# Performance work log

Measured on AMD Instinct MI355X. Metric: run time of the kernel, lower is better.

Reference implementation:

```python
import jax, jax.numpy as jnp
import numpy as np

L = 2          # MPblock_layers
H = 64         # hidden_channels
B, N, E = 1, 50000, 800000


def setup_inputs() -> dict:
    key = jax.random.key(0)
    ks = jax.random.split(key, 12)
    s = 0.05
    return {
        "x": jax.random.normal(ks[0], (B, N, H), jnp.float32),
        "edge_attr": jax.random.normal(ks[1], (B, E, H), jnp.float32),
        "edge_index": jax.random.randint(ks[2], (2, E), 0, N, jnp.int64 if jax.config.jax_enable_x64 else jnp.int32),
        # per-layer stacked MLP params: edge MLP (3H->H->H), node MLP (2H->H->H)
        "edge_w1": jax.random.normal(ks[3], (L, 3 * H, H), jnp.float32) * s,
        "edge_b1": jnp.zeros((L, H), jnp.float32),
        "edge_w2": jax.random.normal(ks[4], (L, H, H), jnp.float32) * s,
        "edge_b2": jnp.zeros((L, H), jnp.float32),
        "node_w1": jax.random.normal(ks[5], (L, 2 * H, H), jnp.float32) * s,
        "node_b1": jnp.zeros((L, H), jnp.float32),
        "node_w2": jax.random.normal(ks[6], (L, H, H), jnp.float32) * s,
        "node_b2": jnp.zeros((L, H), jnp.float32),
    }


def reference(x, edge_attr, edge_index,
              edge_w1, edge_b1, edge_w2, edge_b2,
              node_w1, node_b1, node_w2, node_b2):
    src = edge_index[0]
    dest = edge_index[1]
    n_nodes = x.shape[1]
    for l in range(L):
        # EdgeModel: cat([edge_attr, x[src], x[dest]]) -> MLP
        cat_e = jnp.concatenate([edge_attr, x[:, src], x[:, dest]], axis=2)  # [B,E,3H]
        h = jax.nn.silu(jnp.einsum('bef,fh->beh', cat_e, edge_w1[l]) + edge_b1[l])
        edge_attr = jnp.einsum('beh,hk->bek', h, edge_w2[l]) + edge_b2[l]      # [B,E,H]
        # NodeModel: scatter_add over dest, cat with x, MLP
        agg = jnp.zeros((x.shape[0], n_nodes, edge_attr.shape[2]), x.dtype).at[:, dest].add(edge_attr)
        cat_n = jnp.concatenate([x, agg], axis=2)                              # [B,N,2H]
        h = jax.nn.silu(jnp.einsum('bnf,fh->bnh', cat_n, node_w1[l]) + node_b1[l])
        x = jnp.einsum('bnh,hk->bnk', h, node_w2[l]) + node_b2[l]              # [B,N,H]
    return (x, edge_attr)
```

## Files before the change

### kernel.cpp

```cpp
#include <hip/hip_runtime.h>

typedef __attribute__((ext_vector_type(8))) _Float16 f16x8;
typedef __attribute__((ext_vector_type(4))) _Float16 f16x4;
typedef __attribute__((ext_vector_type(4))) float f32x4;

#define PWS 72

__device__ __forceinline__ float silu_f(float v) {
    return v * (1.0f / (1.0f + __expf(-v)));
}

__device__ __forceinline__ int xcd_swz(int bid, int nwg) {
    if (nwg < 16) return bid;
    int q = nwg >> 3, r = nwg & 7;
    int x = bid & 7, i = bid >> 3;
    int basex = (x < r) ? x * (q + 1) : r * (q + 1) + (x - r) * q;
    return basex + i;
}

struct WDesc { const float* W; _Float16* out; int K; };
struct WPack { WDesc d[8]; };

__global__ __launch_bounds__(256) void conv_weights(WPack p) {
    WDesc wd = p.d[blockIdx.y];
    int total = wd.K * 64;
    int i = blockIdx.x * 256 + threadIdx.x;
    if (i >= total) return;
    int j  = i & 7;
    int l  = (i >> 3) & 63;
    int tn = i >> 9;
    int t  = tn >> 2, nf = tn & 3;
    int k  = t * 32 + (l >> 4) * 8 + j;
    int c  = nf * 16 + (l & 15);
    wd.out[i] = (_Float16)wd.W[k * 64 + c];
}

__global__ __launch_bounds__(256) void hist_kernel(const int* __restrict__ dst,
                                                   int* __restrict__ counts, int E) {
    int e = blockIdx.x * 256 + threadIdx.x;
    if (e < E) atomicAdd(&counts[dst[e]], 1);
}

__global__ __launch_bounds__(1024) void scan_kernel(int* __restrict__ counts,
                                                    int* __restrict__ row_ptr,
                                                    int N, int E) {
    __shared__ int part[1024];
    int t = threadIdx.x;
    int per = (N + 1023) >> 10;
    int s = t * per, en = min(s + per, N);
    int sum = 0;
    for (int i = s; i < en; ++i) sum += counts[i];
    part[t] = sum;
    __syncthreads();
    for (int off = 1; off < 1024; off <<= 1) {
        int v = (t >= off) ? part[t - off] : 0;
        __syncthreads();
        part[t] += v;
        __syncthreads();
    }
    int run = (t == 0) ? 0 : part[t - 1];
    for (int i = s; i < en; ++i) {
        int c = counts[i];
        row_ptr[i] = run;
        counts[i] = run;
        run += c;
    }
    if (t == 1023) row_ptr[N] = E;
}

__global__ __launch_bounds__(256) void scatter_kernel(
    const int* __restrict__ src, const int* __restrict__ dst,
    int* __restrict__ cursor, int4* __restrict__ pk, int E) {
    int e = blockIdx.x * 256 + threadIdx.x;
    if (e < E) {
        int d = dst[e];
        int pos = atomicAdd(&cursor[d], 1);
        pk[pos] = make_int4(e, src[e], d, 0);
    }
}

template <bool IN16, bool FINAL>
__global__ __launch_bounds__(256, 8) void gnn_edge_sorted(
    const float* __restrict__ x,
    const float* __restrict__ ea0,
    _Float16* __restrict__ ea_mid,
    float* __restrict__ ea_out,
    const int4* __restrict__ pk,
    const _Float16* __restrict__ w1f,
    const float* __restrict__ b1,
    const _Float16* __restrict__ w2f,
    const float* __restrict__ b2,
    int E, int nwg)
{
    __shared__ __align__(16) _Float16 sA[64][PWS];

    const int t    = threadIdx.x;
    const int lane = t & 63;
    const int w    = t >> 6;
    const int col  = lane & 15;
    const int g    = lane >> 4;
    const int ko   = g * 8;
    const int bid  = xcd_swz(blockIdx.x, nwg);
    const long base = (long)bid * 64;

    long p0 = base + w * 16 + col;
    if (p0 >= E) p0 = E - 1;
    int ei0 = 0;
    if constexpr (FINAL) ei0 = pk[p0].x;

    f16x4  ea16v[4];
    float4 ea4[4];
    float4 sx4[4], dx4[4];
#pragma unroll
    for (int it = 0; it < 4; ++it) {
        long p = base + w * 16 + it * 4 + g;
        if (p >= E) p = E - 1;
        int4 rec = pk[p];
        if constexpr (IN16) {
            ea16v[it] = *(const f16x4*)(ea_mid + p * 64 + col * 4);
        } else {
            ea4[it] = *(const float4*)(ea0 + (long)rec.x * 64 + col * 4);
        }
        sx4[it] = *(const float4*)(x + (long)rec.y * 64 + col * 4);
        dx4[it] = *(const float4*)(x + (long)rec.z * 64 + col * 4);
    }

    f32x4 acc[4];
#pragma unroll
    for (int nf = 0; nf < 4; ++nf) {
        float bv = b1[nf * 16 + col];
        acc[nf] = (f32x4){bv, bv, bv, bv};
    }

    const int arow = w * 16 + col;

#define MFMA_L1(s3)                                                             \
    _Pragma("unroll")                                                           \
    for (int tt = 0; tt < 2; ++tt) {                                            \
        int k0 = tt * 32 + ko;                                                  \
        f16x8 af = *(const f16x8*)&sA[arow][k0];                                \
        int tg = (s3) * 2 + tt;                                                 \
        _Pragma("unroll")                                                       \
        for (int nf = 0; nf < 4; ++nf) {                                        \
            f16x8 bf = *(const f16x8*)(w1f + (size_t)((tg*4+nf)*64+lane)*8);    \
            acc[nf] = __builtin_amdgcn_mfma_f32_16x16x32_f16(af, bf, acc[nf], 0, 0, 0); \
        }                                                                       \
    }

#pragma unroll
    for (int it = 0; it < 4; ++it) {
        int rg = w * 16 + it * 4 + g;
        f16x4 hv;
        if constexpr (IN16) {
            hv = ea16v[it];
        } else {
            hv[0] = (_Float16)ea4[it].x; hv[1] = (_Float16)ea4[it].y;
            hv[2] = (_Float16)ea4[it].z; hv[3] = (_Float16)ea4[it].w;
        }
        *(f16x4*)&sA[rg][col * 4] = hv;
    }
    MFMA_L1(0)

#pragma unroll
    for (int it = 0; it < 4; ++it) {
        int rg = w * 16 + it * 4 + g;
        f16x4 hv;
        hv[0] = (_Float16)sx4[it].x; hv[1] = (_Float16)sx4[it].y;
        hv[2] = (_Float16)sx4[it].z; hv[3] = (_Float16)sx4[it].w;
        *(f16x4*)&sA[rg][col * 4] = hv;
    }
    MFMA_L1(1)

#pragma unroll
    for (int it = 0; it < 4; ++it) {
        int rg = w * 16 + it * 4 + g;
        f16x4 hv;
        hv[0] = (_Float16)dx4[it].x; hv[1] = (_Float16)dx4[it].y;
        hv[2] = (_Float16)dx4[it].z; hv[3] = (_Float16)dx4[it].w;
        *(f16x4*)&sA[rg][col * 4] = hv;
    }
    MFMA_L1(2)
#undef MFMA_L1

#pragma unroll
    for (int nf = 0; nf < 4; ++nf)
#pragma unroll
        for (int rg = 0; rg < 4; ++rg) {
            int row = w * 16 + g * 4 + rg;
            sA[row][nf * 16 + col] = (_Float16)silu_f(acc[nf][rg]);
        }

    f32x4 out[4];
#pragma unroll
    for (int nf = 0; nf < 4; ++nf) {
        float bv = b2[nf * 16 + col];
        out[nf] = (f32x4){bv, bv, bv, bv};
    }
#pragma unroll
    for (int tt = 0; tt < 2; ++tt) {
        int k0 = tt * 32 + ko;
        f16x8 af = *(const f16x8*)&sA[arow][k0];
#pragma unroll
        for (int nf = 0; nf < 4; ++nf) {
            f16x8 bf = *(const f16x8*)(w2f + (size_t)((tt * 4 + nf) * 64 + lane) * 8);
            out[nf] = __builtin_amdgcn_mfma_f32_16x16x32_f16(af, bf, out[nf], 0, 0, 0);
        }
    }

    const int rbase = w * 16 + g * 4;
#pragma unroll
    for (int rg = 0; rg < 4; ++rg) {
        long p = base + rbase + rg;
        if (p < E) {
#pragma unroll
            for (int nf = 0; nf < 4; ++nf)
                ea_mid[p * 64 + nf * 16 + col] = (_Float16)out[nf][rg];
            if constexpr (FINAL) {
                int eid = __shfl(ei0, g * 4 + rg);
                float* op = ea_out + (long)eid * 64;
#pragma unroll
                for (int nf = 0; nf < 4; ++nf)
                    op[nf * 16 + col] = out[nf][rg];
            }
        }
    }
}

__global__ __launch_bounds__(256, 8) void agg64(
    const _Float16* __restrict__ eaH,
    const int* __restrict__ row_ptr,
    float* __restrict__ agg, int N, int nwg)
{
    const int t    = threadIdx.x;
    const int lane = t & 63;
    const int w    = t >> 6;
    const int col  = lane & 15;
    const int g    = lane >> 4;
    const int bid  = xcd_swz(blockIdx.x, nwg);
    long n = (long)bid * 4 + w;
    if (n >= N) return;

    int pe0 = row_ptr[n], pe1 = row_ptr[n + 1];
    float a0 = 0.f, a1 = 0.f, a2 = 0.f, a3 = 0.f;
    for (int p = pe0 + g; p < pe1; p += 4) {
        f16x4 v = *(const f16x4*)(eaH + (long)p * 64 + col * 4);
        a0 += (float)v[0]; a1 += (float)v[1];
        a2 += (float)v[2]; a3 += (float)v[3];
    }
    a0 += __shfl_xor(a0, 16); a1 += __shfl_xor(a1, 16);
    a2 += __shfl_xor(a2, 16); a3 += __shfl_xor(a3, 16);
    a0 += __shfl_xor(a0, 32); a1 += __shfl_xor(a1, 32);
    a2 += __shfl_xor(a2, 32); a3 += __shfl_xor(a3, 32);
    if (g == 0)
        *(float4*)(agg + n * 64 + col * 4) = make_float4(a0, a1, a2, a3);
}

__global__ __launch_bounds__(256, 8) void gnn_node_mfma(
    const float* __restrict__ x_in,
    const float* __restrict__ aggp,
    float* __restrict__ x_out,
    const _Float16* __restrict__ w1f,
    const float* __restrict__ b1,
    const _Float16* __restrict__ w2f,
    const float* __restrict__ b2, int N)
{
    __shared__ __align__(16) _Float16 sA[64][PWS];

    const int t    = threadIdx.x;
    const int lane = t & 63;
    const int w    = t >> 6;
    const int col  = lane & 15;
    const int g    = lane >> 4;
    const int ko   = g * 8;
    const long base = (long)blockIdx.x * 64;

    long nr = base + w * 16 + col;
    if (nr >= N) nr = N - 1;
    const float* px = x_in + nr * 64 + ko;
    const float* pa = aggp + nr * 64 + ko;

    float4 v0 = *(const float4*)(px);
    float4 v1 = *(const float4*)(px + 4);
    float4 v2 = *(const float4*)(px + 32);
    float4 v3 = *(const float4*)(px + 36);
    float4 v4 = *(const float4*)(pa);
    float4 v5 = *(const float4*)(pa + 4);
    float4 v6 = *(const float4*)(pa + 32);
    float4 v7 = *(const float4*)(pa + 36);

    f32x4 acc[4];
#pragma unroll
    for (int nf = 0; nf < 4; ++nf) {
        float bv = b1[nf * 16 + col];
        acc[nf] = (f32x4){bv, bv, bv, bv};
    }

#define QTR(m, A, B)                                                            \
    {                                                                           \
        f16x8 af;                                                               \
        af[0] = (_Float16)A.x; af[1] = (_Float16)A.y;                           \
        af[2] = (_Float16)A.z; af[3] = (_Float16)A.w;                           \
        af[4] = (_Float16)B.x; af[5] = (_Float16)B.y;                           \
        af[6] = (_Float16)B.z; af[7] = (_Float16)B.w;                           \
        _Pragma("unroll")                                                       \
        for (int nf = 0; nf < 4; ++nf) {                                        \
            f16x8 bf = *(const f16x8*)(w1f + (size_t)(((m)*4+nf)*64+lane)*8);   \
            acc[nf] = __builtin_amdgcn_mfma_f32_16x16x32_f16(af, bf, acc[nf], 0, 0, 0); \
        }                                                                       \
    }
    QTR(0, v0, v1)  QTR(1, v2, v3)
    QTR(2, v4, v5)  QTR(3, v6, v7)
#undef QTR

#pragma unroll
    for (int nf = 0; nf < 4; ++nf)
#pragma unroll
        for (int rg = 0; rg < 4; ++rg) {
            int row = w * 16 + g * 4 + rg;
            sA[row][nf * 16 + col] = (_Float16)silu_f(acc[nf][rg]);
        }

    f32x4 out[4];
#pragma unroll
    for (int nf = 0; nf < 4; ++nf) {
        float bv = b2[nf * 16 + col];
        out[nf] = (f32x4){bv, bv, bv, bv};
    }
    const int arow = w * 16 + col;
#pragma unroll
    for (int tt = 0; tt < 2; ++tt) {
        int k0 = tt * 32 + ko;
        f16x8 af = *(const f16x8*)&sA[arow][k0];
#pragma unroll
        for (int nf = 0; nf < 4; ++nf) {
            f16x8 bf = *(const f16x8*)(w2f + (size_t)((tt * 4 + nf) * 64 + lane) * 8);
            out[nf] = __builtin_amdgcn_mfma_f32_16x16x32_f16(af, bf, out[nf], 0, 0, 0);
        }
    }

    const int rbase = w * 16 + g * 4;
#pragma unroll
    for (int rg = 0; rg < 4; ++rg) {
        long row = base + rbase + rg;
        if (row < N) {
            float* op = x_out + row * 64;
#pragma unroll
            for (int nf = 0; nf < 4; ++nf)
                op[nf * 16 + col] = out[nf][rg];
        }
    }
}

__global__ __launch_bounds__(256, 8) void gnn_edge_mfma(
    const float* __restrict__ x,
    const float* __restrict__ ea_in,
    float* __restrict__ ea_out,
    const int* __restrict__ src_idx,
    const int* __restrict__ dst_idx,
    const _Float16* __restrict__ w1f,
    const float* __restrict__ b1,
    const _Float16* __restrict__ w2f,
    const float* __restrict__ b2,
    float* __restrict__ agg,
    int E)
{
    __shared__ __align__(16) _Float16 sA[64][PWS];

    const int t    = threadIdx.x;
    const int lane = t & 63;
    const int w    = t >> 6;
    const int col  = lane & 15;
    const int g    = lane >> 4;
    const int ko   = g * 8;
    const long base = (long)blockIdx.x * 64;

    long er0 = base + w * 16 + col;
    if (er0 >= E) er0 = E - 1;
    const int di = dst_idx[er0];

    float4 ea4[4], sx4[4], dx4[4];
#pragma unroll
    for (int it = 0; it < 4; ++it) {
        long er = base + w * 16 + it * 4 + g;
        if (er >= E) er = E - 1;
        ea4[it] = *(const float4*)(ea_in + er * 64 + col * 4);
        sx4[it] = *(const float4*)(x + (long)src_idx[er] * 64 + col * 4);
        dx4[it] = *(const float4*)(x + (long)dst_idx[er] * 64 + col * 4);
    }

    f32x4 acc[4];
#pragma unroll
    for (int nf = 0; nf < 4; ++nf) {
        float bv = b1[nf * 16 + col];
        acc[nf] = (f32x4){bv, bv, bv, bv};
    }
    const int arow = w * 16 + col;

#define MFMA_L1(s3)                                                             \
    _Pragma("unroll")                                                           \
    for (int tt = 0; tt < 2; ++tt) {                                            \
        int k0 = tt * 32 + ko;                                                  \
        f16x8 af = *(const f16x8*)&sA[arow][k0];                                \
        int tg = (s3) * 2 + tt;                                                 \
        _Pragma("unroll")                                                       \
        for (int nf = 0; nf < 4; ++nf) {                                        \
            f16x8 bf = *(const f16x8*)(w1f + (size_t)((tg*4+nf)*64+lane)*8);    \
            acc[nf] = __builtin_amdgcn_mfma_f32_16x16x32_f16(af, bf, acc[nf], 0, 0, 0); \
        }                                                                       \
    }

#pragma unroll
    for (int it = 0; it < 4; ++it) {
        int rg = w * 16 + it * 4 + g;
        f16x4 hv;
        hv[0] = (_Float16)ea4[it].x; hv[1] = (_Float16)ea4[it].y;
        hv[2] = (_Float16)ea4[it].z; hv[3] = (_Float16)ea4[it].w;
        *(f16x4*)&sA[rg][col * 4] = hv;
    }
    MFMA_L1(0)
#pragma unroll
    for (int it = 0; it < 4; ++it) {
        int rg = w * 16 + it * 4 + g;
        f16x4 hv;
        hv[0] = (_Float16)sx4[it].x; hv[1] = (_Float16)sx4[it].y;
        hv[2] = (_Float16)sx4[it].z; hv[3] = (_Float16)sx4[it].w;
        *(f16x4*)&sA[rg][col * 4] = hv;
    }
    MFMA_L1(1)
#pragma unroll
    for (int it = 0; it < 4; ++it) {
        int rg = w * 16 + it * 4 + g;
        f16x4 hv;
        hv[0] = (_Float16)dx4[it].x; hv[1] = (_Float16)dx4[it].y;
        hv[2] = (_Float16)dx4[it].z; hv[3] = (_Float16)dx4[it].w;
        *(f16x4*)&sA[rg][col * 4] = hv;
    }
    MFMA_L1(2)
#undef MFMA_L1

#pragma unroll
    for (int nf = 0; nf < 4; ++nf)
#pragma unroll
        for (int rg = 0; rg < 4; ++rg) {
            int row = w * 16 + g * 4 + rg;
            sA[row][nf * 16 + col] = (_Float16)silu_f(acc[nf][rg]);
        }

    f32x4 out[4];
#pragma unroll
    for (int nf = 0; nf < 4; ++nf) {
        float bv = b2[nf * 16 + col];
        out[nf] = (f32x4){bv, bv, bv, bv};
    }
#pragma unroll
    for (int tt = 0; tt < 2; ++tt) {
        int k0 = tt * 32 + ko;
        f16x8 af = *(const f16x8*)&sA[arow][k0];
#pragma unroll
        for (int nf = 0; nf < 4; ++nf) {
            f16x8 bf = *(const f16x8*)(w2f + (size_t)((tt * 4 + nf) * 64 + lane) * 8);
            out[nf] = __builtin_amdgcn_mfma_f32_16x16x32_f16(af, bf, out[nf], 0, 0, 0);
        }
    }

    const int rbase = w * 16 + g * 4;
#pragma unroll
    for (int rg = 0; rg < 4; ++rg) {
        long row = base + rbase + rg;
        if (row < E) {
            int drow = __shfl(di, g * 4 + rg);
            float* ap = agg + (long)drow * 64;
#pragma unroll
            for (int nf = 0; nf < 4; ++nf) {
                ea_out[row * 64 + nf * 16 + col] = out[nf][rg];
                atomicAdd(&ap[nf * 16 + col], out[nf][rg]);
            }
        }
    }
}

extern "C" void kernel_launch(void* const* d_in, const int* in_sizes, int n_in,
                              void* d_out, int out_size, void* d_ws, size_t ws_size,
                              hipStream_t stream) {
    const int H = 64;
    const int N = in_sizes[0] / H;
    const int E = in_sizes[1] / H;

    const float* x0  = (const float*)d_in[0];
    const float* ea0 = (const float*)d_in[1];
    const int*   ei  = (const int*)d_in[2];
    const float* ew1 = (const float*)d_in[3];
    const float* eb1 = (const float*)d_in[4];
    const float* ew2 = (const float*)d_in[5];
    const float* eb2 = (const float*)d_in[6];
    const float* nw1 = (const float*)d_in[7];
    const float* nb1 = (const float*)d_in[8];
    const float* nw2 = (const float*)d_in[9];
    const float* nb2 = (const float*)d_in[10];

    float* outX = (float*)d_out;
    float* outE = outX + (size_t)N * H;

    const size_t aggBytes = (size_t)N * H * sizeof(float);
    const size_t wElems   = 2 * ((size_t)(192 + 64 + 128 + 64) * 64);
    const size_t eaHBytes = (size_t)E * H * sizeof(_Float16);

    float* agg      = (float*)d_ws;
    _Float16* wbase = (_Float16*)((char*)d_ws + aggBytes);
    char* eaH_raw   = (char*)(wbase + wElems);
    eaH_raw = (char*)(((uintptr_t)eaH_raw + 15) & ~(uintptr_t)15);
    _Float16* eaH   = (_Float16*)eaH_raw;
    int* counts     = (int*)(((uintptr_t)((char*)eaH + eaHBytes) + 15) & ~(uintptr_t)15);
    int* row_ptr    = counts + N;
    int4* pk        = (int4*)(((uintptr_t)(row_ptr + N + 1) + 15) & ~(uintptr_t)15);

    const bool sortedOK = ((char*)(pk + E)) <= ((char*)d_ws + ws_size);

    const int* srcI = ei;
    const int* dstI = ei + E;

    WPack pack;
    size_t off = 0;
    _Float16* EW1[2]; _Float16* EW2[2]; _Float16* NW1[2]; _Float16* NW2[2];
    for (int l = 0; l < 2; ++l) {
        EW1[l] = wbase + off; off += 192 * 64;
        EW2[l] = wbase + off; off += 64 * 64;
        NW1[l] = wbase + off; off += 128 * 64;
        NW2[l] = wbase + off; off += 64 * 64;
        pack.d[l * 4 + 0] = {ew1 + (size_t)l * 192 * 64, EW1[l], 192};
        pack.d[l * 4 + 1] = {ew2 + (size_t)l * 64 * 64,  EW2[l], 64};
        pack.d[l * 4 + 2] = {nw1 + (size_t)l * 128 * 64, NW1[l], 128};
        pack.d[l * 4 + 3] = {nw2 + (size_t)l * 64 * 64,  NW2[l], 64};
    }
    conv_weights<<<dim3(48, 8), 256, 0, stream>>>(pack);

    const int egrid = (E + 63) / 64;
    const int ngrid = (N + 63) / 64;
    const int agrid = (N + 3) / 4;

    if (sortedOK) {
        (void)hipMemsetAsync(counts, 0, (size_t)N * sizeof(int), stream);
        hist_kernel<<<(E + 255) / 256, 256, 0, stream>>>(dstI, counts, E);
        scan_kernel<<<1, 1024, 0, stream>>>(counts, row_ptr, N, E);
        scatter_kernel<<<(E + 255) / 256, 256, 0, stream>>>(
            srcI, dstI, counts, pk, E);

        gnn_edge_sorted<false, false><<<egrid, 256, 0, stream>>>(
            x0, ea0, eaH, nullptr, pk,
            EW1[0], eb1, EW2[0], eb2, E, egrid);
        agg64<<<agrid, 256, 0, stream>>>(eaH, row_ptr, agg, N, agrid);
        gnn_node_mfma<<<ngrid, 256, 0, stream>>>(
            x0, agg, outX, NW1[0], nb1, NW2[0], nb2, N);

        gnn_edge_sorted<true, true><<<egrid, 256, 0, stream>>>(
            outX, nullptr, eaH, outE, pk,
            EW1[1], eb1 + H, EW2[1], eb2 + H, E, egrid);
        agg64<<<agrid, 256, 0, stream>>>(eaH, row_ptr, agg, N, agrid);
        gnn_node_mfma<<<ngrid, 256, 0, stream>>>(
            outX, agg, outX, NW1[1], nb1 + H, NW2[1], nb2 + H, N);
    } else {
        for (int l = 0; l < 2; ++l) {
            const float* xin  = (l == 0) ? x0  : outX;
            const float* eain = (l == 0) ? ea0 : outE;
            (void)hipMemsetAsync(agg, 0, aggBytes, stream);
            gnn_edge_mfma<<<egrid, 256, 0, stream>>>(
                xin, eain, outE, srcI, dstI,
                EW1[l], eb1 + l * H, EW2[l], eb2 + l * H, agg, E);
            gnn_node_mfma<<<ngrid, 256, 0, stream>>>(
                xin, agg, outX,
                NW1[l], nb1 + l * H, NW2[l], nb2 + l * H, N);
        }
    }
}
```

Before: 572.3 us.

## Fuse destination aggregation into sorted edge kernel with run-length atomics

Drops the separate agg64 CSR reduction kernel. The sorted edge kernel now accumulates consecutive edges that share a destination in registers and flushes each run to the node aggregate with float atomics, after a memset of agg before each layer. This avoids re-reading the fp16 edge features and one launch per layer. In exchange it adds atomic traffic, makes the sums order-nondeterministic, and accumulates from fp32 outputs where the old path used fp16 values.

```diff
diff --git a/kernel.cpp b/kernel.cpp
--- a/kernel.cpp
+++ b/kernel.cpp
@@ -90,6 +90,7 @@
     const float* __restrict__ b1,
     const _Float16* __restrict__ w2f,
     const float* __restrict__ b2,
+    float* __restrict__ agg,
     int E, int nwg)
 {
     __shared__ __align__(16) _Float16 sA[64][PWS];
@@ -105,8 +106,9 @@
 
     long p0 = base + w * 16 + col;
     if (p0 >= E) p0 = E - 1;
-    int ei0 = 0;
-    if constexpr (FINAL) ei0 = pk[p0].x;
+    const int4 rec0 = pk[p0];
+    const int ei0 = rec0.x;
+    const int d0  = rec0.z;
 
     f16x4  ea16v[4];
     float4 ea4[4];
@@ -208,9 +210,12 @@
     }
 
     const int rbase = w * 16 + g * 4;
+    int dcur = -1;
+    float r0 = 0.f, r1 = 0.f, r2 = 0.f, r3 = 0.f;
 #pragma unroll
     for (int rg = 0; rg < 4; ++rg) {
         long p = base + rbase + rg;
+        int dn = __shfl(d0, g * 4 + rg);
         if (p < E) {
 #pragma unroll
             for (int nf = 0; nf < 4; ++nf)
@@ -222,37 +227,27 @@
                 for (int nf = 0; nf < 4; ++nf)
                     op[nf * 16 + col] = out[nf][rg];
             }
-        }
-    }
-}
-
-__global__ __launch_bounds__(256, 8) void agg64(
-    const _Float16* __restrict__ eaH,
-    const int* __restrict__ row_ptr,
-    float* __restrict__ agg, int N, int nwg)
-{
-    const int t    = threadIdx.x;
-    const int lane = t & 63;
-    const int w    = t >> 6;
-    const int col  = lane & 15;
-    const int g    = lane >> 4;
-    const int bid  = xcd_swz(blockIdx.x, nwg);
-    long n = (long)bid * 4 + w;
-    if (n >= N) return;
-
-    int pe0 = row_ptr[n], pe1 = row_ptr[n + 1];
-    float a0 = 0.f, a1 = 0.f, a2 = 0.f, a3 = 0.f;
-    for (int p = pe0 + g; p < pe1; p += 4) {
-        f16x4 v = *(const f16x4*)(eaH + (long)p * 64 + col * 4);
-        a0 += (float)v[0]; a1 += (float)v[1];
-        a2 += (float)v[2]; a3 += (float)v[3];
-    }
-    a0 += __shfl_xor(a0, 16); a1 += __shfl_xor(a1, 16);
-    a2 += __shfl_xor(a2, 16); a3 += __shfl_xor(a3, 16);
-    a0 += __shfl_xor(a0, 32); a1 += __shfl_xor(a1, 32);
-    a2 += __shfl_xor(a2, 32); a3 += __shfl_xor(a3, 32);
-    if (g == 0)
-        *(float4*)(agg + n * 64 + col * 4) = make_float4(a0, a1, a2, a3);
+            if (dn != dcur) {
+                if (dcur >= 0) {
+                    float* ap = agg + (long)dcur * 64;
+                    atomicAdd(&ap[col],      r0);
+                    atomicAdd(&ap[16 + col], r1);
+                    atomicAdd(&ap[32 + col], r2);
+                    atomicAdd(&ap[48 + col], r3);
+                }
+                dcur = dn; r0 = r1 = r2 = r3 = 0.f;
+            }
+            r0 += out[0][rg]; r1 += out[1][rg];
+            r2 += out[2][rg]; r3 += out[3][rg];
+        }
+    }
+    if (dcur >= 0) {
+        float* ap = agg + (long)dcur * 64;
+        atomicAdd(&ap[col],      r0);
+        atomicAdd(&ap[16 + col], r1);
+        atomicAdd(&ap[32 + col], r2);
+        atomicAdd(&ap[48 + col], r3);
+    }
 }
 
 __global__ __launch_bounds__(256, 8) void gnn_node_mfma(
@@ -536,7 +531,6 @@
 
     const int egrid = (E + 63) / 64;
     const int ngrid = (N + 63) / 64;
-    const int agrid = (N + 3) / 4;
 
     if (sortedOK) {
         (void)hipMemsetAsync(counts, 0, (size_t)N * sizeof(int), stream);
@@ -545,17 +539,17 @@
         scatter_kernel<<<(E + 255) / 256, 256, 0, stream>>>(
             srcI, dstI, counts, pk, E);
 
+        (void)hipMemsetAsync(agg, 0, aggBytes, stream);
         gnn_edge_sorted<false, false><<<egrid, 256, 0, stream>>>(
             x0, ea0, eaH, nullptr, pk,
-            EW1[0], eb1, EW2[0], eb2, E, egrid);
-        agg64<<<agrid, 256, 0, stream>>>(eaH, row_ptr, agg, N, agrid);
+            EW1[0], eb1, EW2[0], eb2, agg, E, egrid);
         gnn_node_mfma<<<ngrid, 256, 0, stream>>>(
             x0, agg, outX, NW1[0], nb1, NW2[0], nb2, N);
 
+        (void)hipMemsetAsync(agg, 0, aggBytes, stream);
         gnn_edge_sorted<true, true><<<egrid, 256, 0, stream>>>(
             outX, nullptr, eaH, outE, pk,
-            EW1[1], eb1 + H, EW2[1], eb2 + H, E, egrid);
-        agg64<<<agrid, 256, 0, stream>>>(eaH, row_ptr, agg, N, agrid);
+            EW1[1], eb1 + H, EW2[1], eb2 + H, agg, E, egrid);
         gnn_node_mfma<<<ngrid, 256, 0, stream>>>(
             outX, agg, outX, NW1[1], nb1 + H, NW2[1], nb2 + H, N);
     } else {
```

Result: slower. 711.2 us (+24.3%).
